# Optimization experiments

Hardware: AMD Instinct MI355X
Metric: run time of the kernel (lower is better)

Reference implementation:

```python
import math
import jax, jax.numpy as jnp
import numpy as np


def _tril_colmajor_index(d):
    # Maps packed icf tail entries (column-by-column, strictly lower) to (r, c).
    idx = np.zeros((d, d), dtype=np.int32)
    p = 0
    for c in range(d):
        for r in range(c + 1, d):
            idx[r, c] = p
            p += 1
    mask = np.tri(d, d, -1, dtype=bool)  # strictly lower triangular
    return idx, mask


def setup_inputs() -> dict:
    key = jax.random.key(0)
    k1, k2, k3, k4 = jax.random.split(key, 4)
    K, d, N = 64, 32, 50000
    icf_cols = d + d * (d - 1) // 2  # 528
    return {
        "alphas": jax.random.normal(k1, (K,), dtype=jnp.float32),
        "means": jax.random.normal(k2, (K, d), dtype=jnp.float32),
        "icf": jax.random.normal(k3, (K, icf_cols), dtype=jnp.float32),
        "x": jax.random.normal(k4, (N, d), dtype=jnp.float32),
        "wishart_gamma": jnp.ones((), dtype=jnp.float32),
        "wishart_m": jnp.ones((), dtype=jnp.float32),
    }


def reference(alphas, means, icf, x, wishart_gamma, wishart_m):
    n, d = x.shape
    k = alphas.shape[0]
    idx, mask = _tril_colmajor_index(d)
    idx = jnp.asarray(idx)
    mask = jnp.asarray(mask)

    Qdiags = jnp.exp(icf[:, :d])            # [K, d]
    sum_qs = jnp.sum(icf[:, :d], axis=1)    # [K]
    Ltail = icf[:, d:]                      # [K, d(d-1)/2]
    # Vectorized constructL: strictly-lower triangular L per component. [K, d, d]
    L = jnp.where(mask[None], Ltail[:, idx], jnp.zeros((), icf.dtype))

    xc = x[:, None, :] - means[None, :, :]  # [N, K, d]
    # Qtimesx: diag scaling + batched triangular matvec
    Lx = Qdiags[None] * xc + jnp.einsum('kij,nkj->nki', L, xc)  # [N, K, d]
    sqsum = jnp.sum(Lx * Lx, axis=2)        # [N, K]

    inner = alphas[None, :] + sum_qs[None, :] - 0.5 * sqsum
    slse = jnp.sum(jax.scipy.special.logsumexp(inner, axis=1))

    CONSTANT = -n * d * 0.5 * math.log(2 * math.pi)

    # log_wishart_prior
    nw = d + wishart_m + 1.0
    out_w = jnp.sum(0.5 * wishart_gamma * wishart_gamma
                    * (jnp.sum(Qdiags ** 2, axis=1) + jnp.sum(Ltail ** 2, axis=1))
                    - wishart_m * sum_qs)
    C = nw * d * jnp.log(wishart_gamma / math.sqrt(2.0))
    prior = out_w - k * (C - jax.scipy.special.multigammaln(0.5 * nw, d))

    return CONSTANT + slse - n * jax.scipy.special.logsumexp(alphas) + prior
```

## Files before the change

kernel.cpp:

```cpp
#include <hip/hip_runtime.h>
#include <hip/hip_bf16.h>
#include <math.h>
#include <utility>

#define K_COMP 64
#define D 32
#define NTRIL 496
#define ICF_COLS 528
#define NPAIR 528
#define NFEAT 560
#define NCHUNK 18
#define PTS_PER_BLK 32
#define ROWB 1168
#define XSTRIDE 33

typedef __attribute__((ext_vector_type(8))) short v8s;
typedef __attribute__((ext_vector_type(4))) float v4f;

__device__ __forceinline__ unsigned short f2bf(float f) {
  unsigned int u = __float_as_uint(f);
  unsigned int r = (u + 0x7FFFu + ((u >> 16) & 1u)) >> 16;
  return (unsigned short)r;
}
__device__ __forceinline__ v8s asv8(int4 v) {
  union { int4 i; v8s s; } u; u.i = v; return u.s;
}

constexpr int pr_i(int t) { int i = 0; while (t >= D - i) { t -= D - i; ++i; } return i; }
constexpr int pr_j(int t) { int i = 0; while (t >= D - i) { t -= D - i; ++i; } return i + t; }

template<int F> __device__ __forceinline__ float featL(const float* __restrict__ xrow) {
  if constexpr (F < 32) return xrow[F];
  else if constexpr (F < NFEAT) {
    constexpr int t = F - 32, i = pr_i(t), j = pr_j(t);
    return xrow[i] * xrow[j];
  } else return 0.0f;
}

template<int F0> __device__ __forceinline__ void write4L(const float* __restrict__ xrow, char* row) {
  __hip_bfloat162 pa = __float22bfloat162_rn(make_float2(featL<F0+0>(xrow), featL<F0+1>(xrow)));
  __hip_bfloat162 pb = __float22bfloat162_rn(make_float2(featL<F0+2>(xrow), featL<F0+3>(xrow)));
  union { __hip_bfloat162 h2; unsigned u; } ua, ub;
  ua.h2 = pa; ub.h2 = pb;
  *reinterpret_cast<uint2*>(row + (size_t)F0 * 2) = make_uint2(ua.u, ub.u);
}
template<int BASE, size_t... Qs> __device__ __forceinline__
void gen72(const float* __restrict__ xrow, char* row, std::index_sequence<Qs...>) {
  (write4L<BASE + 4 * (int)Qs>(xrow, row), ...);
}

__global__ __launch_bounds__(64) void gmm_prep(
    const float* __restrict__ alphas, const float* __restrict__ means,
    const float* __restrict__ icf, const float* __restrict__ wg,
    const float* __restrict__ wm,
    uint4* __restrict__ Whi, float* __restrict__ eSa, float* __restrict__ wwk)
{
  int k = blockIdx.x;
  int l = threadIdx.x;
  __shared__ float M[D][D + 1];
  __shared__ float mu[D], b[D], v[D];
  __shared__ float At[NPAIR];
  __shared__ float red[64];

  const float* ick = icf + (size_t)k * ICF_COLS;

  if (l < D) {
    mu[l] = means[k * D + l];
    float q = __expf(ick[l]);
    for (int c = 0; c < D; ++c) {
      float val;
      if (c < l) { int off = c * 31 - c * (c - 1) / 2; val = ick[D + off + (l - c - 1)]; }
      else if (c == l) val = q;
      else val = 0.0f;
      M[l][c] = val;
    }
  }
  __syncthreads();
  if (l < D) {
    float acc = 0.f;
    for (int c = 0; c < D; ++c) acc = fmaf(M[l][c], mu[c], acc);
    b[l] = acc;
  }
  __syncthreads();
  if (l < D) {
    float acc = 0.f;
    for (int r = 0; r < D; ++r) acc = fmaf(M[r][l], b[r], acc);
    v[l] = acc;
  }
  for (int t = l; t < NPAIR; t += 64) {
    int tt = t, i = 0;
    while (tt >= D - i) { tt -= D - i; ++i; }
    int j = i + tt;
    float acc = 0.f;
    for (int r = 0; r < D; ++r) acc = fmaf(M[r][i], M[r][j], acc);
    At[t] = (i == j) ? -0.5f * acc : -acc;
  }
  float part = 0.f;
  for (int e = l; e < D * D; e += 64) {
    float mv = M[e / D][e % D];
    part = fmaf(mv, mv, part);
  }
  red[l] = part;
  __syncthreads();
  for (int st = 32; st > 0; st >>= 1) {
    if (l < st) red[l] += red[l + st];
    __syncthreads();
  }
  if (l == 0) {
    float msq = red[0];
    float sumq = 0.f;
    for (int i = 0; i < D; ++i) sumq += ick[i];
    float bsq = 0.f;
    for (int i = 0; i < D; ++i) bsq = fmaf(b[i], b[i], bsq);
    eSa[k] = alphas[k] + sumq - 0.5f * bsq;
    float g = wg[0], mm = wm[0];
    wwk[k] = 0.5f * g * g * msq - mm * sumq;
  }
  __syncthreads();

  int s = k >> 4, krow = k & 15;
  for (int u = l; u < NCHUNK * 4; u += 64) {
    int c = u >> 2, g = u & 3;
    unsigned int hw[4] = {0, 0, 0, 0};
    for (int j2 = 0; j2 < 8; ++j2) {
      int f = c * 32 + g * 8 + j2;
      float wv2;
      if (f < 32) wv2 = v[f];
      else if (f < NFEAT) wv2 = At[f - 32];
      else wv2 = 0.0f;
      hw[j2 >> 1] |= ((unsigned int)f2bf(wv2)) << (16 * (j2 & 1));
    }
    Whi[(s * NCHUNK + c) * 64 + g * 16 + krow] = make_uint4(hw[0], hw[1], hw[2], hw[3]);
  }
}

__global__ __launch_bounds__(256, 4) void gmm_main(
    const float* __restrict__ x, const int4* __restrict__ Whi,
    const float* __restrict__ eSa, int N, float* __restrict__ partials)
{
  __shared__ __align__(16) char phi[PTS_PER_BLK * ROWB];
  __shared__ float xs[PTS_PER_BLK][XSTRIDE];
  __shared__ float lmm[4][PTS_PER_BLK];
  __shared__ float lss[4][PTS_PER_BLK];

  int tid = threadIdx.x;
  int lane = tid & 63;
  int slice = __builtin_amdgcn_readfirstlane(tid >> 6);
  int g = lane >> 4, n16 = lane & 15;

  {
    size_t fidx = (size_t)blockIdx.x * (PTS_PER_BLK * D) + tid * 4;
    size_t maxf = (size_t)N * D - 4;
    if (fidx > maxf) fidx = maxf;
    float4 v = *reinterpret_cast<const float4*>(x + fidx);
    int r = tid >> 3, c = (tid & 7) * 4;
    xs[r][c + 0] = v.x; xs[r][c + 1] = v.y; xs[r][c + 2] = v.z; xs[r][c + 3] = v.w;
  }
  __syncthreads();

  {
    int ptl = tid & 31;
    int h = tid >> 5;
    const float* xrow = &xs[ptl][0];
    char* row = phi + (size_t)ptl * ROWB;
    switch (h) {
      case 0: gen72<  0>(xrow, row, std::make_index_sequence<18>{}); break;
      case 1: gen72< 72>(xrow, row, std::make_index_sequence<18>{}); break;
      case 2: gen72<144>(xrow, row, std::make_index_sequence<18>{}); break;
      case 3: gen72<216>(xrow, row, std::make_index_sequence<18>{}); break;
      case 4: gen72<288>(xrow, row, std::make_index_sequence<18>{}); break;
      case 5: gen72<360>(xrow, row, std::make_index_sequence<18>{}); break;
      case 6: gen72<432>(xrow, row, std::make_index_sequence<18>{}); break;
      case 7: gen72<504>(xrow, row, std::make_index_sequence<18>{}); break;
    }
  }
  __syncthreads();

  v4f acc0 = {0.f, 0.f, 0.f, 0.f};
  v4f acc1 = {0.f, 0.f, 0.f, 0.f};
  const char* brow0 = phi + (size_t)(0 * 16 + n16) * ROWB + g * 16;
  const char* brow1 = phi + (size_t)(1 * 16 + n16) * ROWB + g * 16;
  const int4* wp = Whi + slice * NCHUNK * 64 + lane;

  int4 ah = wp[0];
#pragma unroll
  for (int c = 0; c < NCHUNK; ++c) {
    int4 ah_n;
    if (c + 1 < NCHUNK) ah_n = wp[(c + 1) * 64];
    int4 b0 = *reinterpret_cast<const int4*>(brow0 + c * 64);
    int4 b1 = *reinterpret_cast<const int4*>(brow1 + c * 64);
    v8s ahs = asv8(ah), b0s = asv8(b0), b1s = asv8(b1);
    acc0 = __builtin_amdgcn_mfma_f32_16x16x32_bf16(ahs, b0s, acc0, 0, 0, 0);
    acc1 = __builtin_amdgcn_mfma_f32_16x16x32_bf16(ahs, b1s, acc1, 0, 0, 0);
    ah = ah_n;
  }

  float4 es = reinterpret_cast<const float4*>(eSa)[slice * 4 + g];
  acc0.x += es.x; acc0.y += es.y; acc0.z += es.z; acc0.w += es.w;
  acc1.x += es.x; acc1.y += es.y; acc1.z += es.z; acc1.w += es.w;

#pragma unroll
  for (int G = 0; G < 2; ++G) {
    v4f a = (G == 0) ? acc0 : acc1;
    float m = fmaxf(fmaxf(a.x, a.y), fmaxf(a.z, a.w));
    float sv = __expf(a.x - m) + __expf(a.y - m) + __expf(a.z - m) + __expf(a.w - m);
#pragma unroll
    for (int off = 16; off <= 32; off <<= 1) {
      float mo = __shfl_xor(m, off);
      float so = __shfl_xor(sv, off);
      float mn = fmaxf(m, mo);
      sv = sv * __expf(m - mn) + so * __expf(mo - mn);
      m = mn;
    }
    if (lane < 16) { lmm[slice][G * 16 + lane] = m; lss[slice][G * 16 + lane] = sv; }
  }
  __syncthreads();

  if (tid < PTS_PER_BLK) {
    float m0 = lmm[0][tid], m1 = lmm[1][tid], m2 = lmm[2][tid], m3 = lmm[3][tid];
    float mm = fmaxf(fmaxf(m0, m1), fmaxf(m2, m3));
    float ss = lss[0][tid] * __expf(m0 - mm) + lss[1][tid] * __expf(m1 - mm)
             + lss[2][tid] * __expf(m2 - mm) + lss[3][tid] * __expf(m3 - mm);
    int n = blockIdx.x * PTS_PER_BLK + tid;
    float lse = (n < N) ? (mm + __logf(ss)) : 0.f;
#pragma unroll
    for (int off = 16; off > 0; off >>= 1) lse += __shfl_down(lse, off);
    if (tid == 0) partials[blockIdx.x] = lse;
  }
}

__global__ __launch_bounds__(256) void gmm_final(
    const float* __restrict__ wwk, const float* __restrict__ partials, int nblocks,
    const float* __restrict__ alphas, const float* __restrict__ wg,
    const float* __restrict__ wm, int N, float* __restrict__ out)
{
  int tid = threadIdx.x;
  __shared__ double sd[256];
  __shared__ float samax;
  __shared__ double s_slse, s_sa, s_ow;

  double acc = 0.0;
  for (int i = tid; i < nblocks; i += 256) acc += (double)partials[i];
  sd[tid] = acc;
  __syncthreads();
  for (int st = 128; st > 0; st >>= 1) {
    if (tid < st) sd[tid] += sd[tid + st];
    __syncthreads();
  }
  if (tid == 0) s_slse = sd[0];
  __syncthreads();

  if (tid < 64) {
    float m = alphas[tid];
#pragma unroll
    for (int off = 32; off > 0; off >>= 1) m = fmaxf(m, __shfl_xor(m, off));
    if (tid == 0) samax = m;
  }
  __syncthreads();

  sd[tid] = (tid < K_COMP) ? exp((double)(alphas[tid] - samax)) : 0.0;
  __syncthreads();
  for (int st = 128; st > 0; st >>= 1) {
    if (tid < st) sd[tid] += sd[tid + st];
    __syncthreads();
  }
  if (tid == 0) s_sa = sd[0];
  __syncthreads();

  sd[tid] = (tid < K_COMP) ? (double)wwk[tid] : 0.0;
  __syncthreads();
  for (int st = 128; st > 0; st >>= 1) {
    if (tid < st) sd[tid] += sd[tid + st];
    __syncthreads();
  }
  if (tid == 0) s_ow = sd[0];
  __syncthreads();

  double nw = (double)D + (double)wm[0] + 1.0;
  sd[tid] = (tid < D) ? lgamma(0.5 * nw + (1.0 - (double)(tid + 1)) * 0.5) : 0.0;
  __syncthreads();
  for (int st = 128; st > 0; st >>= 1) {
    if (tid < st) sd[tid] += sd[tid + st];
    __syncthreads();
  }

  if (tid == 0) {
    double mg = (D * (D - 1) / 4.0) * log(M_PI) + sd[0];
    double lse_a = (double)samax + log(s_sa);
    double g = (double)wg[0];
    double C = nw * (double)D * log(g / sqrt(2.0));
    double CONST = -(double)N * D * 0.5 * log(2.0 * M_PI);
    double prior = s_ow - (double)K_COMP * (C - mg);
    out[0] = (float)(CONST + s_slse - (double)N * lse_a + prior);
  }
}

extern "C" void kernel_launch(void* const* d_in, const int* in_sizes, int n_in,
                              void* d_out, int out_size, void* d_ws, size_t ws_size,
                              hipStream_t stream)
{
  const float* alphas = (const float*)d_in[0];
  const float* means  = (const float*)d_in[1];
  const float* icf    = (const float*)d_in[2];
  const float* x      = (const float*)d_in[3];
  const float* wg     = (const float*)d_in[4];
  const float* wm     = (const float*)d_in[5];
  float* out = (float*)d_out;

  int N = in_sizes[3] / D;
  int npblk = (N + PTS_PER_BLK - 1) / PTS_PER_BLK;

  char* wsb = (char*)d_ws;
  const size_t WBYTES = (size_t)4 * NCHUNK * 64 * 16;
  uint4* Whi = (uint4*)wsb;
  float* eSa = (float*)(wsb + WBYTES);
  float* wwk = eSa + K_COMP;
  float* partials = wwk + K_COMP;

  gmm_prep<<<K_COMP, 64, 0, stream>>>(alphas, means, icf, wg, wm, Whi, eSa, wwk);
  gmm_main<<<npblk, 256, 0, stream>>>(x, (const int4*)Whi, eSa, N, partials);
  gmm_final<<<1, 256, 0, stream>>>(wwk, partials, npblk, alphas, wg, wm, N, out);
}
```

Measured before the change: 39.95 us.

## Fuse final reduction into main kernel via last-block atomic counter

```diff
diff --git a/kernel.cpp b/kernel.cpp
--- a/kernel.cpp
+++ b/kernel.cpp
@@ -52,8 +52,9 @@
 __global__ __launch_bounds__(64) void gmm_prep(
     const float* __restrict__ alphas, const float* __restrict__ means,
     const float* __restrict__ icf, const float* __restrict__ wg,
-    const float* __restrict__ wm,
-    uint4* __restrict__ Whi, float* __restrict__ eSa, float* __restrict__ wwk)
+    const float* __restrict__ wm, int N,
+    uint4* __restrict__ Whi, float* __restrict__ eSa, float* __restrict__ wwk,
+    double* __restrict__ tailc)
 {
   int k = blockIdx.x;
   int l = threadIdx.x;
@@ -132,16 +133,44 @@
     }
     Whi[(s * NCHUNK + c) * 64 + g * 16 + krow] = make_uint4(hw[0], hw[1], hw[2], hw[3]);
   }
+
+  if (k == 0) {
+    float a = alphas[l];
+    float m = a;
+#pragma unroll
+    for (int off = 32; off > 0; off >>= 1) m = fmaxf(m, __shfl_xor(m, off));
+    double e = exp((double)(a - m));
+#pragma unroll
+    for (int off = 32; off > 0; off >>= 1) e += __shfl_xor(e, off);
+    double lse_a = (double)m + log(e);
+
+    double nw = (double)D + (double)wm[0] + 1.0;
+    double lg = (l < D) ? lgamma(0.5 * nw + (1.0 - (double)(l + 1)) * 0.5) : 0.0;
+#pragma unroll
+    for (int off = 32; off > 0; off >>= 1) lg += __shfl_xor(lg, off);
+
+    if (l == 0) {
+      double mg = (D * (D - 1) / 4.0) * log(M_PI) + lg;
+      double gg = (double)wg[0];
+      double C = nw * (double)D * log(gg / sqrt(2.0));
+      double CONST = -(double)N * D * 0.5 * log(2.0 * M_PI);
+      tailc[0] = CONST - (double)N * lse_a - (double)K_COMP * (C - mg);
+    }
+  }
 }
 
 __global__ __launch_bounds__(256, 4) void gmm_main(
     const float* __restrict__ x, const int4* __restrict__ Whi,
-    const float* __restrict__ eSa, int N, float* __restrict__ partials)
+    const float* __restrict__ eSa, const float* __restrict__ wwk,
+    const double* __restrict__ tailc, int N,
+    float* __restrict__ partials, unsigned int* __restrict__ counter,
+    float* __restrict__ out)
 {
   __shared__ __align__(16) char phi[PTS_PER_BLK * ROWB];
   __shared__ float xs[PTS_PER_BLK][XSTRIDE];
   __shared__ float lmm[4][PTS_PER_BLK];
   __shared__ float lss[4][PTS_PER_BLK];
+  __shared__ unsigned int isLastS;
 
   int tid = threadIdx.x;
   int lane = tid & 63;
@@ -227,71 +256,29 @@
     for (int off = 16; off > 0; off >>= 1) lse += __shfl_down(lse, off);
     if (tid == 0) partials[blockIdx.x] = lse;
   }
-}
-
-__global__ __launch_bounds__(256) void gmm_final(
-    const float* __restrict__ wwk, const float* __restrict__ partials, int nblocks,
-    const float* __restrict__ alphas, const float* __restrict__ wg,
-    const float* __restrict__ wm, int N, float* __restrict__ out)
-{
-  int tid = threadIdx.x;
-  __shared__ double sd[256];
-  __shared__ float samax;
-  __shared__ double s_slse, s_sa, s_ow;
-
-  double acc = 0.0;
-  for (int i = tid; i < nblocks; i += 256) acc += (double)partials[i];
-  sd[tid] = acc;
-  __syncthreads();
-  for (int st = 128; st > 0; st >>= 1) {
-    if (tid < st) sd[tid] += sd[tid + st];
+
+  if (tid == 0) {
+    __threadfence();
+    isLastS = (atomicAdd(counter, 1u) == gridDim.x - 1) ? 1u : 0u;
+  }
+  __syncthreads();
+  if (isLastS == 0) return;
+  __threadfence();
+
+  {
+    int nblocks = gridDim.x;
+    double* sd = reinterpret_cast<double*>(phi);
+    volatile const float* vp = partials;
+    double acc = 0.0;
+    for (int i = tid; i < nblocks; i += 256) acc += (double)vp[i];
+    if (tid < K_COMP) acc += (double)wwk[tid];
+    sd[tid] = acc;
     __syncthreads();
-  }
-  if (tid == 0) s_slse = sd[0];
-  __syncthreads();
-
-  if (tid < 64) {
-    float m = alphas[tid];
-#pragma unroll
-    for (int off = 32; off > 0; off >>= 1) m = fmaxf(m, __shfl_xor(m, off));
-    if (tid == 0) samax = m;
-  }
-  __syncthreads();
-
-  sd[tid] = (tid < K_COMP) ? exp((double)(alphas[tid] - samax)) : 0.0;
-  __syncthreads();
-  for (int st = 128; st > 0; st >>= 1) {
-    if (tid < st) sd[tid] += sd[tid + st];
-    __syncthreads();
-  }
-  if (tid == 0) s_sa = sd[0];
-  __syncthreads();
-
-  sd[tid] = (tid < K_COMP) ? (double)wwk[tid] : 0.0;
-  __syncthreads();
-  for (int st = 128; st > 0; st >>= 1) {
-    if (tid < st) sd[tid] += sd[tid + st];
-    __syncthreads();
-  }
-  if (tid == 0) s_ow = sd[0];
-  __syncthreads();
-
-  double nw = (double)D + (double)wm[0] + 1.0;
-  sd[tid] = (tid < D) ? lgamma(0.5 * nw + (1.0 - (double)(tid + 1)) * 0.5) : 0.0;
-  __syncthreads();
-  for (int st = 128; st > 0; st >>= 1) {
-    if (tid < st) sd[tid] += sd[tid + st];
-    __syncthreads();
-  }
-
-  if (tid == 0) {
-    double mg = (D * (D - 1) / 4.0) * log(M_PI) + sd[0];
-    double lse_a = (double)samax + log(s_sa);
-    double g = (double)wg[0];
-    double C = nw * (double)D * log(g / sqrt(2.0));
-    double CONST = -(double)N * D * 0.5 * log(2.0 * M_PI);
-    double prior = s_ow - (double)K_COMP * (C - mg);
-    out[0] = (float)(CONST + s_slse - (double)N * lse_a + prior);
+    for (int st = 128; st > 0; st >>= 1) {
+      if (tid < st) sd[tid] += sd[tid + st];
+      __syncthreads();
+    }
+    if (tid == 0) out[0] = (float)(sd[0] + tailc[0]);
   }
 }
 
@@ -312,12 +299,15 @@
 
   char* wsb = (char*)d_ws;
   const size_t WBYTES = (size_t)4 * NCHUNK * 64 * 16;
-  uint4* Whi = (uint4*)wsb;
-  float* eSa = (float*)(wsb + WBYTES);
-  float* wwk = eSa + K_COMP;
-  float* partials = wwk + K_COMP;
-
-  gmm_prep<<<K_COMP, 64, 0, stream>>>(alphas, means, icf, wg, wm, Whi, eSa, wwk);
-  gmm_main<<<npblk, 256, 0, stream>>>(x, (const int4*)Whi, eSa, N, partials);
-  gmm_final<<<1, 256, 0, stream>>>(wwk, partials, npblk, alphas, wg, wm, N, out);
-}
+  uint4*  Whi = (uint4*)wsb;
+  float*  eSa = (float*)(wsb + WBYTES);
+  float*  wwk = eSa + K_COMP;
+  double* tailc = (double*)(wsb + WBYTES + 512);
+  float*  partials = (float*)(wsb + WBYTES + 512 + 8);
+  unsigned int* counter = (unsigned int*)(partials + npblk);
+
+  hipMemsetAsync(counter, 0, sizeof(unsigned int), stream);
+  gmm_prep<<<K_COMP, 64, 0, stream>>>(alphas, means, icf, wg, wm, N, Whi, eSa, wwk, tailc);
+  gmm_main<<<npblk, 256, 0, stream>>>(x, (const int4*)Whi, eSa, wwk, tailc, N,
+                                      partials, counter, out);
+}
```

Result: slower. 68.68 us (+71.9%).
